# Optimization experiments

Measured on AMD Instinct MI355X. Metric: run time of the kernel, lower is better.

## Reference

```python
import jax, jax.numpy as jnp
import numpy as np

D_MODEL = 1024
N_HEADS = 16
D_K = 64
SEQ = 4096
BATCH = 1


def setup_inputs() -> dict:
    key = jax.random.key(0)
    ks = jax.random.split(key, 6)
    s = 1.0 / np.sqrt(D_MODEL)
    return {
        "h": jax.random.normal(ks[0], (BATCH, SEQ, D_MODEL), jnp.float32),
        "gamma": jnp.ones((D_MODEL,), jnp.float32),
        "beta": jnp.zeros((D_MODEL,), jnp.float32),
        "Wq": jax.random.normal(ks[1], (D_MODEL, N_HEADS * D_K), jnp.float32) * s,
        "bq": jnp.zeros((N_HEADS * D_K,), jnp.float32),
        "Wk": jax.random.normal(ks[2], (D_MODEL, N_HEADS * D_K), jnp.float32) * s,
        "bk": jnp.zeros((N_HEADS * D_K,), jnp.float32),
        "Wv": jax.random.normal(ks[3], (D_MODEL, N_HEADS * D_K), jnp.float32) * s,
        "bv": jnp.zeros((N_HEADS * D_K,), jnp.float32),
        "Wo": jax.random.normal(ks[4], (N_HEADS * D_K, D_MODEL), jnp.float32) * s,
        "bo": jnp.zeros((D_MODEL,), jnp.float32),
    }


def _rope(x):
    # x: [b, s, h, d]
    d = x.shape[-1]
    d2 = d // 2
    theta = 1.0 / (10000.0 ** (jnp.arange(0, d, 2, dtype=jnp.float32) / d))  # [d2]
    pos = jnp.arange(x.shape[1], dtype=jnp.float32)  # [s]
    idx_theta = pos[:, None] * theta[None, :]  # [s, d2]
    idx_theta2 = jnp.concatenate([idx_theta, idx_theta], axis=-1)  # [s, d]
    cos = jnp.cos(idx_theta2)[None, :, None, :]
    sin = jnp.sin(idx_theta2)[None, :, None, :]
    neg_half = jnp.concatenate([-x[..., d2:], x[..., :d2]], axis=-1)
    return x * cos + neg_half * sin


def reference(h, gamma, beta, Wq, bq, Wk, bk, Wv, bv, Wo, bo):
    b, s, dm = h.shape
    h_res = h
    # LayerNorm (eps=1e-5, matching torch default)
    mu = jnp.mean(h, axis=-1, keepdims=True)
    var = jnp.var(h, axis=-1, keepdims=True)
    hn = (h - mu) * jax.lax.rsqrt(var + 1e-5) * gamma + beta
    mh = (b, s, N_HEADS, D_K)
    q = (hn @ Wq + bq).reshape(mh)
    k = (hn @ Wk + bk).reshape(mh)
    v = (hn @ Wv + bv).reshape(mh)
    q = _rope(q)
    k = _rope(k)
    scale = 1.0 / np.sqrt(D_K)
    attn = jnp.einsum('bihd,bjhd->bhij', q, k) * scale  # [b,h,s,s]
    # causal mask
    mask = jnp.tril(jnp.ones((s, s), dtype=bool))
    attn = jnp.where(mask, attn, -jnp.inf)
    attn = jax.nn.softmax(attn, axis=-1)
    out = jnp.einsum('bhij,bjhd->bihd', attn, v).reshape(b, s, N_HEADS * D_K)
    return out @ Wo + bo + h_res
```

## Files before the change

kernel.cpp:

```cpp
#include <hip/hip_runtime.h>
#include <stdint.h>

#define SEQLEN 4096
#define DMODEL 1024
#define NHEADS 16
#define DKDIM  64

typedef unsigned short u16;
typedef unsigned int   u32;
using f32x4 = __attribute__((ext_vector_type(4))) float;
using i32x4 = __attribute__((ext_vector_type(4))) int;
using i32x2 = __attribute__((ext_vector_type(2))) int;
using u16x8 = __attribute__((ext_vector_type(8))) unsigned short;

__device__ __forceinline__ u16 f2bf(float f) {
    u32 x = __builtin_bit_cast(u32, f);
    u32 r = x + 0x7fffu + ((x >> 16) & 1u);
    return (u16)(r >> 16);
}
__device__ __forceinline__ float exp2a(float x) {
    float r; asm("v_exp_f32 %0, %1" : "=v"(r) : "v"(x)); return r;
}
__device__ __forceinline__ u32 cvtpk(float lo, float hi) {
    u32 r; asm("v_cvt_pk_bf16_f32 %0, %1, %2" : "=v"(r) : "v"(lo), "v"(hi)); return r;
}

__device__ __forceinline__ void mfma_bf16(f32x4& d, i32x4 a, i32x4 b) {
    asm("v_mfma_f32_16x16x32_bf16 %0, %1, %2, %0" : "+v"(d) : "v"(a), "v"(b));
}
__device__ __forceinline__ void mfma16_bf16(f32x4& d, i32x2 a, i32x2 b) {
    asm("v_mfma_f32_16x16x16_bf16 %0, %1, %2, %0" : "+v"(d) : "v"(a), "v"(b));
}

#define ASYNC_COPY16(gsrc, ldst) \
    __builtin_amdgcn_global_load_lds((const __attribute__((address_space(1))) void*)(gsrc), \
                                     (__attribute__((address_space(3))) void*)(ldst), 16, 0, 0)

__global__ __launch_bounds__(256) void ln_kernel(const float* __restrict__ h,
                                                 const float* __restrict__ gamma,
                                                 const float* __restrict__ beta,
                                                 u16* __restrict__ hn) {
    int row = blockIdx.x;
    int t = threadIdx.x;
    float4 v = reinterpret_cast<const float4*>(h + (size_t)row * DMODEL)[t];
    float s  = v.x + v.y + v.z + v.w;
    float s2 = v.x*v.x + v.y*v.y + v.z*v.z + v.w*v.w;
#pragma unroll
    for (int off = 1; off < 64; off <<= 1) {
        s  += __shfl_xor(s, off);
        s2 += __shfl_xor(s2, off);
    }
    __shared__ float red[8];
    int wid = t >> 6, lane = t & 63;
    if (lane == 0) { red[wid] = s; red[4 + wid] = s2; }
    __syncthreads();
    s  = red[0] + red[1] + red[2] + red[3];
    s2 = red[4] + red[5] + red[6] + red[7];
    float mu   = s * (1.0f / DMODEL);
    float rstd = rsqrtf(s2 * (1.0f / DMODEL) - mu * mu + 1e-5f);
    float4 g = reinterpret_cast<const float4*>(gamma)[t];
    float4 b = reinterpret_cast<const float4*>(beta)[t];
    ushort4 o;
    o.x = f2bf((v.x - mu) * rstd * g.x + b.x);
    o.y = f2bf((v.y - mu) * rstd * g.y + b.y);
    o.z = f2bf((v.z - mu) * rstd * g.z + b.z);
    o.w = f2bf((v.w - mu) * rstd * g.w + b.w);
    reinterpret_cast<ushort4*>(hn + (size_t)row * DMODEL)[t] = o;
}

__global__ __launch_bounds__(256) void wconv_kernel(const float* __restrict__ Wq,
                                                    const float* __restrict__ Wk,
                                                    const float* __restrict__ Wv,
                                                    const float* __restrict__ Wo,
                                                    u16* __restrict__ wqkvT,
                                                    u16* __restrict__ woT) {
    int z = blockIdx.z;
    const float* W = (z == 0) ? Wq : (z == 1) ? Wk : (z == 2) ? Wv : Wo;
    u16* Wt = (z < 3) ? wqkvT + (size_t)z * DMODEL * DMODEL : woT;
    __shared__ float tile[32][33];
    int bx = blockIdx.x * 32;
    int by = blockIdx.y * 32;
    int tx = threadIdx.x & 31, ty = threadIdx.x >> 5;
#pragma unroll
    for (int i = 0; i < 32; i += 8)
        tile[ty + i][tx] = W[(size_t)(by + ty + i) * DMODEL + bx + tx];
    __syncthreads();
#pragma unroll
    for (int i = 0; i < 32; i += 8)
        Wt[(size_t)(bx + ty + i) * DMODEL + by + tx] = f2bf(tile[tx][ty + i]);
}

__global__ void rope_table_kernel(float* __restrict__ cosT, float* __restrict__ sinT) {
    int idx = blockIdx.x * 256 + threadIdx.x;
    int s = idx >> 5, i = idx & 31;
    float theta = powf(10000.0f, -2.0f * (float)i / 64.0f);
    float ang = (float)s * theta;
    cosT[idx] = cosf(ang);
    sinT[idx] = sinf(ang);
}

template <int EPI>
__global__ __launch_bounds__(256) void gemm_kernel(const u16* __restrict__ A,
                                                   const u16* __restrict__ Bt,
                                                   const float* __restrict__ b0,
                                                   const float* __restrict__ b1,
                                                   const float* __restrict__ b2,
                                                   const float* __restrict__ resid,
                                                   const float* __restrict__ cosT,
                                                   const float* __restrict__ sinT,
                                                   u16* __restrict__ o0,
                                                   u16* __restrict__ o1,
                                                   u16* __restrict__ o2,
                                                   float* __restrict__ ofp) {
    __shared__ alignas(16) u16 As[2][128 * 64];
    __shared__ alignas(16) u16 Bs[2][128 * 64];
    int bm = blockIdx.x, bn = blockIdx.y;
    int tid = threadIdx.x;
    int wid = tid >> 6, lane = tid & 63;
    int wm = wid >> 1, wn = wid & 1;
    int t15 = lane & 15, g = lane >> 4;
    const u16* Abase = A  + (size_t)bm * 128 * DMODEL;
    const u16* Bbase = Bt + (size_t)bn * 128 * DMODEL;
    int srow = tid >> 3;
    int sslot = tid & 7;
    f32x4 acc[4][4] = {};

#define GSTAGE(b, ks)                                                                    \
    {                                                                                    \
        _Pragma("unroll")                                                                \
        for (int i = 0; i < 4; i++) {                                                    \
            int row = i * 32 + srow;                                                     \
            int col = ((sslot ^ (row & 7)) * 8) + (ks);                                  \
            ASYNC_COPY16(Abase + (size_t)row * DMODEL + col, &As[b][i * 2048 + wid * 512]); \
            ASYNC_COPY16(Bbase + (size_t)row * DMODEL + col, &Bs[b][i * 2048 + wid * 512]); \
        }                                                                                \
    }

    GSTAGE(0, 0)
    __syncthreads();
    int buf = 0;
    for (int ks = 0; ks < DMODEL; ks += 64) {
        if (ks < DMODEL - 64) GSTAGE(buf ^ 1, ks + 64)
#pragma unroll
        for (int kk = 0; kk < 2; kk++) {
            i32x4 af[4], bfr[4];
#pragma unroll
            for (int mi = 0; mi < 4; mi++) {
                int row = wm * 64 + mi * 16 + t15;
                int sl = (kk * 4 + g) ^ (row & 7);
                af[mi] = *reinterpret_cast<const i32x4*>(&As[buf][row * 64 + sl * 8]);
            }
#pragma unroll
            for (int ni = 0; ni < 4; ni++) {
                int row = wn * 64 + ni * 16 + t15;
                int sl = (kk * 4 + g) ^ (row & 7);
                bfr[ni] = *reinterpret_cast<const i32x4*>(&Bs[buf][row * 64 + sl * 8]);
            }
            __builtin_amdgcn_s_setprio(1);
#pragma unroll
            for (int mi = 0; mi < 4; mi++)
#pragma unroll
                for (int ni = 0; ni < 4; ni++)
                    mfma_bf16(acc[mi][ni], af[mi], bfr[ni]);
            __builtin_amdgcn_s_setprio(0);
        }
        __syncthreads();
        buf ^= 1;
    }
#undef GSTAGE

    if (EPI == 0) {
        int seg = bn >> 3;
        int bnl = bn & 7;
        const float* bias = (seg == 0) ? b0 : (seg == 1) ? b1 : b2;
        if (seg < 2) {
            u16* o = (seg == 0) ? o0 : o1;
            float qs = (seg == 0) ? 0.18033688f : 1.0f;
#pragma unroll
            for (int mi = 0; mi < 4; mi++) {
#pragma unroll
                for (int nl = 0; nl < 2; nl++) {
                    int n10 = bnl * 128 + wn * 64 + nl * 16 + t15;
                    int head = n10 >> 6;
                    int dA = n10 & 63, dB = dA + 32;
                    float bvA = bias[n10], bvB = bias[n10 + 32];
#pragma unroll
                    for (int r = 0; r < 4; r++) {
                        int m = bm * 128 + wm * 64 + mi * 16 + g * 4 + r;
                        float c  = cosT[m * 32 + dA];
                        float sn = sinT[m * 32 + dA];
                        float xA = acc[mi][nl][r] + bvA;
                        float xB = acc[mi][nl + 2][r] + bvB;
                        o[(size_t)(head * SEQLEN + m) * DKDIM + dA] = f2bf((xA * c - xB * sn) * qs);
                        o[(size_t)(head * SEQLEN + m) * DKDIM + dB] = f2bf((xB * c + xA * sn) * qs);
                    }
                }
            }
        } else {
#pragma unroll
            for (int mi = 0; mi < 4; mi++) {
#pragma unroll
                for (int ni = 0; ni < 4; ni++) {
                    int n10 = bnl * 128 + wn * 64 + ni * 16 + t15;
                    int head = n10 >> 6, dv = n10 & 63;
                    float bv = bias[n10];
                    int m = bm * 128 + wm * 64 + mi * 16 + g * 4;
                    ushort4 w4;
                    w4.x = f2bf(acc[mi][ni][0] + bv);
                    w4.y = f2bf(acc[mi][ni][1] + bv);
                    w4.z = f2bf(acc[mi][ni][2] + bv);
                    w4.w = f2bf(acc[mi][ni][3] + bv);
                    *reinterpret_cast<ushort4*>(&o2[(size_t)(head * DKDIM + dv) * SEQLEN + m]) = w4;
                }
            }
        }
    } else {
#pragma unroll
        for (int mi = 0; mi < 4; mi++) {
#pragma unroll
            for (int ni = 0; ni < 4; ni++) {
                int n = bn * 128 + wn * 64 + ni * 16 + t15;
                float bv = b0[n];
#pragma unroll
                for (int r = 0; r < 4; r++) {
                    int m = bm * 128 + wm * 64 + mi * 16 + g * 4 + r;
                    ofp[(size_t)m * DMODEL + n] = acc[mi][ni][r] + bv + resid[(size_t)m * DMODEL + n];
                }
            }
        }
    }
}

__global__ __launch_bounds__(512, 2) void attn_kernel(const u16* __restrict__ q,
                                                      const u16* __restrict__ k,
                                                      const u16* __restrict__ vt,
                                                      u16* __restrict__ o) {
    __shared__ alignas(16) u16 SMEM[65536];
    int bid = blockIdx.x;
    int h = bid & 15;
    int p = bid >> 4;
    int tid = threadIdx.x;
    int grp = tid >> 8;
    int wid = (tid >> 6) & 3;
    int lane = tid & 63;
    int t15 = lane & 15, g = lane >> 4;
    const u16* Qh  = q  + (size_t)h * SEQLEN * DKDIM;
    const u16* Kh  = k  + (size_t)h * SEQLEN * DKDIM;
    const u16* VtH = vt + (size_t)h * DKDIM * SEQLEN;
    int sslotK = lane & 7;
    int sslotV = lane & 15;
    float* Os  = (float*)SMEM;
    float2* Ml = (float2*)((char*)SMEM + 69632);

    int c7 = t15 & 7;
    int kc0e = t15 * 64 + ((g ^ c7) << 3);
    int kc1e = t15 * 64 + (((4 + g) ^ c7) << 3);
    int vce[8];
#pragma unroll
    for (int kb = 0; kb < 8; kb++)
        vce[kb] = t15 * 128 + ((((kb * 2) + (g >> 1)) ^ c7) << 3) + ((g & 1) << 2);

#define STAGE(bb, t_)                                                                   \
    {                                                                                   \
        int k0s = (t_) * 128;                                                           \
        u16* Kb = SMEM + (size_t)(grp * 2 + (bb)) * 8192;                               \
        u16* Vb = SMEM + 32768 + (size_t)(grp * 2 + (bb)) * 8192;                       \
        _Pragma("unroll")                                                               \
        for (int it = 0; it < 4; it++) {                                                \
            int u    = wid * 4 + it;                                                    \
            int krow = u * 8 + (lane >> 3);                                             \
            int ksl  = (sslotK ^ (krow & 7)) * 8;                                       \
            ASYNC_COPY16(Kh + (size_t)(k0s + krow) * DKDIM + ksl, Kb + u * 512);        \
            int vrow = u * 4 + (lane >> 4);                                             \
            int vsl  = (sslotV ^ (vrow & 7)) * 8;                                       \
            ASYNC_COPY16(VtH + (size_t)vrow * SEQLEN + k0s + vsl, Vb + u * 512);        \
        }                                                                               \
    }

    for (int pass = 0; pass < 2; pass++) {
        int Q = pass ? p : (31 - p);
        int n = Q + 1;
        int iters = (n + 1) >> 1;
        int q0 = Q * 128;
        int qrowA = q0 + wid * 32 + t15;
        int qrowB = qrowA + 16;
        i32x4 qfA0, qfA1, qfB0, qfB1;
        {
            const u16* qp = Qh + (size_t)qrowA * DKDIM + g * 8;
            qfA0 = *reinterpret_cast<const i32x4*>(qp);
            qfA1 = *reinterpret_cast<const i32x4*>(qp + 32);
            const u16* qp2 = qp + 16 * DKDIM;
            qfB0 = *reinterpret_cast<const i32x4*>(qp2);
            qfB1 = *reinterpret_cast<const i32x4*>(qp2 + 32);
        }
        f32x4 oA[4] = {}, oB[4] = {};
        float mA = -1e30f, mB = -1e30f, lA = 0.f, lB = 0.f;

        if (grp < n) STAGE(0, grp)
        __syncthreads();
        for (int i = 0; i < iters; i++) {
            int t = grp + 2 * i;
            bool active = t < n;
            int buf = i & 1;
            if (t + 2 < n) STAGE(buf ^ 1, t + 2)
            if (active) {
                int kbe = (grp * 2 + buf) * 8192;
                const u16* Kp0 = SMEM + kbe + kc0e;
                const u16* Kp1 = SMEM + kbe + kc1e;
                const u16* Vp  = SMEM + 32768 + kbe;
                int k0 = t * 128;
                f32x4 sA[8] = {}, sB[8] = {};
                __builtin_amdgcn_s_setprio(1);
#pragma unroll
                for (int kb = 0; kb < 8; kb++) {
                    i32x4 kf0 = *reinterpret_cast<const i32x4*>(Kp0 + kb * 1024);
                    i32x4 kf1 = *reinterpret_cast<const i32x4*>(Kp1 + kb * 1024);
                    mfma_bf16(sA[kb], kf0, qfA0);
                    mfma_bf16(sA[kb], kf1, qfA1);
                    mfma_bf16(sB[kb], kf0, qfB0);
                    mfma_bf16(sB[kb], kf1, qfB1);
                }
                __builtin_amdgcn_s_setprio(0);
                if (t == n - 1) {
#pragma unroll
                    for (int kb = 0; kb < 8; kb++)
#pragma unroll
                        for (int r = 0; r < 4; r++) {
                            int kvg = k0 + kb * 16 + g * 4 + r;
                            if (kvg > qrowA) sA[kb][r] = -1e30f;
                            if (kvg > qrowB) sB[kb][r] = -1e30f;
                        }
                }
                float amx[8], bmx[8];
#pragma unroll
                for (int kb = 0; kb < 8; kb++) {
                    amx[kb] = fmaxf(fmaxf(sA[kb][0], sA[kb][1]), fmaxf(sA[kb][2], sA[kb][3]));
                    bmx[kb] = fmaxf(fmaxf(sB[kb][0], sB[kb][1]), fmaxf(sB[kb][2], sB[kb][3]));
                }
                float mxA = fmaxf(fmaxf(fmaxf(amx[0], amx[1]), fmaxf(amx[2], amx[3])),
                                  fmaxf(fmaxf(amx[4], amx[5]), fmaxf(amx[6], amx[7])));
                float mxB = fmaxf(fmaxf(fmaxf(bmx[0], bmx[1]), fmaxf(bmx[2], bmx[3])),
                                  fmaxf(fmaxf(bmx[4], bmx[5]), fmaxf(bmx[6], bmx[7])));
                if (!__all((mxA <= mA + 8.0f) && (mxB <= mB + 8.0f))) {
                    float mrA = fmaxf(mxA, __shfl_xor(mxA, 16));
                    mrA = fmaxf(mrA, __shfl_xor(mrA, 32));
                    float mnA = fmaxf(mA, mrA);
                    float fdA = exp2a(mA - mnA);
                    mA = mnA; lA *= fdA;
                    oA[0] *= fdA; oA[1] *= fdA; oA[2] *= fdA; oA[3] *= fdA;
                    float mrB = fmaxf(mxB, __shfl_xor(mxB, 16));
                    mrB = fmaxf(mrB, __shfl_xor(mrB, 32));
                    float mnB = fmaxf(mB, mrB);
                    float fdB = exp2a(mB - mnB);
                    mB = mnB; lB *= fdB;
                    oB[0] *= fdB; oB[1] *= fdB; oB[2] *= fdB; oB[3] *= fdB;
                }
                float psA = 0.f, psB = 0.f;
                u32 pwA[16], pwB[16];
#pragma unroll
                for (int kb = 0; kb < 8; kb++) {
                    float pa0 = exp2a(sA[kb][0] - mA);
                    float pa1 = exp2a(sA[kb][1] - mA);
                    float pa2 = exp2a(sA[kb][2] - mA);
                    float pa3 = exp2a(sA[kb][3] - mA);
                    psA += (pa0 + pa1) + (pa2 + pa3);
                    pwA[kb * 2]     = cvtpk(pa0, pa1);
                    pwA[kb * 2 + 1] = cvtpk(pa2, pa3);
                    float pb0 = exp2a(sB[kb][0] - mB);
                    float pb1 = exp2a(sB[kb][1] - mB);
                    float pb2 = exp2a(sB[kb][2] - mB);
                    float pb3 = exp2a(sB[kb][3] - mB);
                    psB += (pb0 + pb1) + (pb2 + pb3);
                    pwB[kb * 2]     = cvtpk(pb0, pb1);
                    pwB[kb * 2 + 1] = cvtpk(pb2, pb3);
                }
                lA += psA;
                lB += psB;
                __builtin_amdgcn_s_setprio(1);
#pragma unroll
                for (int nb = 0; nb < 4; nb++) {
#pragma unroll
                    for (int kb = 0; kb < 8; kb++) {
                        i32x2 vf = *reinterpret_cast<const i32x2*>(Vp + vce[kb] + nb * 2048);
                        mfma16_bf16(oA[nb], vf, i32x2{(int)pwA[kb * 2], (int)pwA[kb * 2 + 1]});
                        mfma16_bf16(oB[nb], vf, i32x2{(int)pwB[kb * 2], (int)pwB[kb * 2 + 1]});
                    }
                }
                __builtin_amdgcn_s_setprio(0);
            }
            __syncthreads();
        }
        lA += __shfl_xor(lA, 16); lA += __shfl_xor(lA, 32);
        lB += __shfl_xor(lB, 16); lB += __shfl_xor(lB, 32);
        int rowA = wid * 32 + t15, rowB = rowA + 16;
#pragma unroll
        for (int nb = 0; nb < 4; nb++) {
            *reinterpret_cast<f32x4*>(&Os[(size_t)(grp * 128 + rowA) * 68 + nb * 16 + g * 4]) = oA[nb];
            *reinterpret_cast<f32x4*>(&Os[(size_t)(grp * 128 + rowB) * 68 + nb * 16 + g * 4]) = oB[nb];
        }
        if (g == 0) {
            Ml[grp * 128 + rowA] = make_float2(mA, lA);
            Ml[grp * 128 + rowB] = make_float2(mB, lB);
        }
        __syncthreads();
        {
            int r = tid >> 2, c4 = tid & 3;
            int d0 = c4 * 16;
            float2 c0 = Ml[r], c1 = Ml[128 + r];
            float M = fmaxf(c0.x, c1.x);
            float w0 = exp2a(c0.x - M), w1 = exp2a(c1.x - M);
            float invL = 1.0f / (w0 * c0.y + w1 * c1.y);
            u16* op = o + (size_t)(q0 + r) * DMODEL + h * DKDIM + d0;
#pragma unroll
            for (int j = 0; j < 2; j++) {
                f32x4 a0 = *reinterpret_cast<const f32x4*>(&Os[(size_t)r * 68 + d0 + j * 8]);
                f32x4 a1 = *reinterpret_cast<const f32x4*>(&Os[(size_t)r * 68 + d0 + j * 8 + 4]);
                f32x4 b0 = *reinterpret_cast<const f32x4*>(&Os[(size_t)(128 + r) * 68 + d0 + j * 8]);
                f32x4 b1 = *reinterpret_cast<const f32x4*>(&Os[(size_t)(128 + r) * 68 + d0 + j * 8 + 4]);
                u16x8 w8;
#pragma unroll
                for (int ii = 0; ii < 4; ii++) {
                    w8[ii]     = f2bf((w0 * a0[ii] + w1 * b0[ii]) * invL);
                    w8[4 + ii] = f2bf((w0 * a1[ii] + w1 * b1[ii]) * invL);
                }
                *reinterpret_cast<u16x8*>(op + j * 8) = w8;
            }
        }
        __syncthreads();
    }
#undef STAGE
}

extern "C" void kernel_launch(void* const* d_in, const int* in_sizes, int n_in,
                              void* d_out, int out_size, void* d_ws, size_t ws_size,
                              hipStream_t stream) {
    const float* h     = (const float*)d_in[0];
    const float* gamma = (const float*)d_in[1];
    const float* beta  = (const float*)d_in[2];
    const float* Wq    = (const float*)d_in[3];
    const float* bq    = (const float*)d_in[4];
    const float* Wk    = (const float*)d_in[5];
    const float* bk    = (const float*)d_in[6];
    const float* Wv    = (const float*)d_in[7];
    const float* bv    = (const float*)d_in[8];
    const float* Wo    = (const float*)d_in[9];
    const float* bo    = (const float*)d_in[10];
    float* out = (float*)d_out;

    char* ws = (char*)d_ws;
    u16* hn     = (u16*)(ws);
    u16* wqkvT  = (u16*)(ws + (8ull  << 20));
    u16* woT    = (u16*)(ws + (14ull << 20));
    u16* qb     = (u16*)(ws + (16ull << 20));
    u16* kbuf   = (u16*)(ws + (24ull << 20));
    u16* vtb    = (u16*)(ws + (32ull << 20));
    float* cosT = (float*)(ws + (40ull << 20));
    float* sinT = (float*)(ws + (40ull << 20) + (512ull << 10));
    u16* attn = hn;

    ln_kernel<<<SEQLEN, 256, 0, stream>>>(h, gamma, beta, hn);
    wconv_kernel<<<dim3(32, 32, 4), 256, 0, stream>>>(Wq, Wk, Wv, Wo, wqkvT, woT);
    rope_table_kernel<<<(SEQLEN * 32) / 256, 256, 0, stream>>>(cosT, sinT);
    gemm_kernel<0><<<dim3(32, 24), 256, 0, stream>>>(hn, wqkvT, bq, bk, bv, nullptr,
                                                     cosT, sinT, qb, kbuf, vtb, nullptr);
    attn_kernel<<<256, 512, 0, stream>>>(qb, kbuf, vtb, attn);
    gemm_kernel<1><<<dim3(32, 8), 256, 0, stream>>>(attn, woT, bo, nullptr, nullptr, h,
                                                    nullptr, nullptr, nullptr, nullptr, nullptr, out);
}
```

Before: 136.6 us.

## Merge prep kernels into one launch and interleave softmax with PV MFMAs

Combines the LayerNorm, weight transpose/convert and RoPE table kernels into a single prep kernel that dispatches on block index, removing two kernel launches and their serialization gaps. In the attention inner loop, each packed bf16 P fragment now feeds its PV MFMAs as soon as it is produced, instead of all exponentials finishing before any MFMA starts. This shortens the live range of the P register arrays and lets exp work overlap with matrix ops, at the cost of more frequent priority toggles and per-kb V fragment loads interleaved with ALU work.

After: 132.9 us. 1.03x faster.

```diff
diff --git a/kernel.cpp b/kernel.cpp
--- a/kernel.cpp
+++ b/kernel.cpp
@@ -36,67 +36,70 @@
     __builtin_amdgcn_global_load_lds((const __attribute__((address_space(1))) void*)(gsrc), \
                                      (__attribute__((address_space(3))) void*)(ldst), 16, 0, 0)
 
-__global__ __launch_bounds__(256) void ln_kernel(const float* __restrict__ h,
-                                                 const float* __restrict__ gamma,
-                                                 const float* __restrict__ beta,
-                                                 u16* __restrict__ hn) {
-    int row = blockIdx.x;
+__global__ __launch_bounds__(256) void prep_kernel(const float* __restrict__ Wq,
+                                                   const float* __restrict__ Wk,
+                                                   const float* __restrict__ Wv,
+                                                   const float* __restrict__ Wo,
+                                                   u16* __restrict__ wqkvT,
+                                                   u16* __restrict__ woT,
+                                                   const float* __restrict__ h,
+                                                   const float* __restrict__ gamma,
+                                                   const float* __restrict__ beta,
+                                                   u16* __restrict__ hn,
+                                                   float* __restrict__ cosT,
+                                                   float* __restrict__ sinT) {
+    __shared__ float tile[32][33];
+    __shared__ float red[8];
+    int bid = blockIdx.x;
     int t = threadIdx.x;
-    float4 v = reinterpret_cast<const float4*>(h + (size_t)row * DMODEL)[t];
-    float s  = v.x + v.y + v.z + v.w;
-    float s2 = v.x*v.x + v.y*v.y + v.z*v.z + v.w*v.w;
-#pragma unroll
-    for (int off = 1; off < 64; off <<= 1) {
-        s  += __shfl_xor(s, off);
-        s2 += __shfl_xor(s2, off);
-    }
-    __shared__ float red[8];
-    int wid = t >> 6, lane = t & 63;
-    if (lane == 0) { red[wid] = s; red[4 + wid] = s2; }
-    __syncthreads();
-    s  = red[0] + red[1] + red[2] + red[3];
-    s2 = red[4] + red[5] + red[6] + red[7];
-    float mu   = s * (1.0f / DMODEL);
-    float rstd = rsqrtf(s2 * (1.0f / DMODEL) - mu * mu + 1e-5f);
-    float4 g = reinterpret_cast<const float4*>(gamma)[t];
-    float4 b = reinterpret_cast<const float4*>(beta)[t];
-    ushort4 o;
-    o.x = f2bf((v.x - mu) * rstd * g.x + b.x);
-    o.y = f2bf((v.y - mu) * rstd * g.y + b.y);
-    o.z = f2bf((v.z - mu) * rstd * g.z + b.z);
-    o.w = f2bf((v.w - mu) * rstd * g.w + b.w);
-    reinterpret_cast<ushort4*>(hn + (size_t)row * DMODEL)[t] = o;
-}
-
-__global__ __launch_bounds__(256) void wconv_kernel(const float* __restrict__ Wq,
-                                                    const float* __restrict__ Wk,
-                                                    const float* __restrict__ Wv,
-                                                    const float* __restrict__ Wo,
-                                                    u16* __restrict__ wqkvT,
-                                                    u16* __restrict__ woT) {
-    int z = blockIdx.z;
-    const float* W = (z == 0) ? Wq : (z == 1) ? Wk : (z == 2) ? Wv : Wo;
-    u16* Wt = (z < 3) ? wqkvT + (size_t)z * DMODEL * DMODEL : woT;
-    __shared__ float tile[32][33];
-    int bx = blockIdx.x * 32;
-    int by = blockIdx.y * 32;
-    int tx = threadIdx.x & 31, ty = threadIdx.x >> 5;
-#pragma unroll
-    for (int i = 0; i < 32; i += 8)
-        tile[ty + i][tx] = W[(size_t)(by + ty + i) * DMODEL + bx + tx];
-    __syncthreads();
-#pragma unroll
-    for (int i = 0; i < 32; i += 8)
-        Wt[(size_t)(bx + ty + i) * DMODEL + by + tx] = f2bf(tile[tx][ty + i]);
-}
-
-__global__ void rope_table_kernel(float* __restrict__ cosT, float* __restrict__ sinT) {
-    int idx = blockIdx.x * 256 + threadIdx.x;
-    int s = idx >> 5, i = idx & 31;
-    float theta = powf(10000.0f, -2.0f * (float)i / 64.0f);
-    float ang = (float)s * theta;
-    cosT[idx] = cosf(ang);
-    sinT[idx] = sinf(ang);
+    if (bid < 4096) {
+        int z = bid >> 10;
+        int rem = bid & 1023;
+        const float* W = (z == 0) ? Wq : (z == 1) ? Wk : (z == 2) ? Wv : Wo;
+        u16* Wt = (z < 3) ? wqkvT + (size_t)z * DMODEL * DMODEL : woT;
+        int bx = (rem & 31) * 32;
+        int by = (rem >> 5) * 32;
+        int tx = t & 31, ty = t >> 5;
+#pragma unroll
+        for (int i = 0; i < 32; i += 8)
+            tile[ty + i][tx] = W[(size_t)(by + ty + i) * DMODEL + bx + tx];
+        __syncthreads();
+#pragma unroll
+        for (int i = 0; i < 32; i += 8)
+            Wt[(size_t)(bx + ty + i) * DMODEL + by + tx] = f2bf(tile[tx][ty + i]);
+    } else if (bid < 8192) {
+        int row = bid - 4096;
+        float4 v = reinterpret_cast<const float4*>(h + (size_t)row * DMODEL)[t];
+        float s  = v.x + v.y + v.z + v.w;
+        float s2 = v.x*v.x + v.y*v.y + v.z*v.z + v.w*v.w;
+#pragma unroll
+        for (int off = 1; off < 64; off <<= 1) {
+            s  += __shfl_xor(s, off);
+            s2 += __shfl_xor(s2, off);
+        }
+        int wid = t >> 6, lane = t & 63;
+        if (lane == 0) { red[wid] = s; red[4 + wid] = s2; }
+        __syncthreads();
+        s  = red[0] + red[1] + red[2] + red[3];
+        s2 = red[4] + red[5] + red[6] + red[7];
+        float mu   = s * (1.0f / DMODEL);
+        float rstd = rsqrtf(s2 * (1.0f / DMODEL) - mu * mu + 1e-5f);
+        float4 g = reinterpret_cast<const float4*>(gamma)[t];
+        float4 b = reinterpret_cast<const float4*>(beta)[t];
+        ushort4 o;
+        o.x = f2bf((v.x - mu) * rstd * g.x + b.x);
+        o.y = f2bf((v.y - mu) * rstd * g.y + b.y);
+        o.z = f2bf((v.z - mu) * rstd * g.z + b.z);
+        o.w = f2bf((v.w - mu) * rstd * g.w + b.w);
+        reinterpret_cast<ushort4*>(hn + (size_t)row * DMODEL)[t] = o;
+    } else {
+        int idx = (bid - 8192) * 256 + t;
+        int s = idx >> 5, i = idx & 31;
+        float theta = powf(10000.0f, -2.0f * (float)i / 64.0f);
+        float ang = (float)s * theta;
+        cosT[idx] = cosf(ang);
+        sinT[idx] = sinf(ang);
+    }
 }
 
 template <int EPI>
@@ -356,7 +359,6 @@
                     oB[0] *= fdB; oB[1] *= fdB; oB[2] *= fdB; oB[3] *= fdB;
                 }
                 float psA = 0.f, psB = 0.f;
-                u32 pwA[16], pwB[16];
 #pragma unroll
                 for (int kb = 0; kb < 8; kb++) {
                     float pa0 = exp2a(sA[kb][0] - mA);
@@ -364,29 +366,24 @@
                     float pa2 = exp2a(sA[kb][2] - mA);
                     float pa3 = exp2a(sA[kb][3] - mA);
                     psA += (pa0 + pa1) + (pa2 + pa3);
-                    pwA[kb * 2]     = cvtpk(pa0, pa1);
-                    pwA[kb * 2 + 1] = cvtpk(pa2, pa3);
+                    i32x2 pfA = i32x2{(int)cvtpk(pa0, pa1), (int)cvtpk(pa2, pa3)};
                     float pb0 = exp2a(sB[kb][0] - mB);
                     float pb1 = exp2a(sB[kb][1] - mB);
                     float pb2 = exp2a(sB[kb][2] - mB);
                     float pb3 = exp2a(sB[kb][3] - mB);
                     psB += (pb0 + pb1) + (pb2 + pb3);
-                    pwB[kb * 2]     = cvtpk(pb0, pb1);
-                    pwB[kb * 2 + 1] = cvtpk(pb2, pb3);
+                    i32x2 pfB = i32x2{(int)cvtpk(pb0, pb1), (int)cvtpk(pb2, pb3)};
+                    __builtin_amdgcn_s_setprio(1);
+#pragma unroll
+                    for (int nb = 0; nb < 4; nb++) {
+                        i32x2 vf = *reinterpret_cast<const i32x2*>(Vp + vce[kb] + nb * 2048);
+                        mfma16_bf16(oA[nb], vf, pfA);
+                        mfma16_bf16(oB[nb], vf, pfB);
+                    }
+                    __builtin_amdgcn_s_setprio(0);
                 }
                 lA += psA;
                 lB += psB;
-                __builtin_amdgcn_s_setprio(1);
-#pragma unroll
-                for (int nb = 0; nb < 4; nb++) {
-#pragma unroll
-                    for (int kb = 0; kb < 8; kb++) {
-                        i32x2 vf = *reinterpret_cast<const i32x2*>(Vp + vce[kb] + nb * 2048);
-                        mfma16_bf16(oA[nb], vf, i32x2{(int)pwA[kb * 2], (int)pwA[kb * 2 + 1]});
-                        mfma16_bf16(oB[nb], vf, i32x2{(int)pwB[kb * 2], (int)pwB[kb * 2 + 1]});
-                    }
-                }
-                __builtin_amdgcn_s_setprio(0);
             }
             __syncthreads();
         }
@@ -458,9 +455,8 @@
     float* sinT = (float*)(ws + (40ull << 20) + (512ull << 10));
     u16* attn = hn;
 
-    ln_kernel<<<SEQLEN, 256, 0, stream>>>(h, gamma, beta, hn);
-    wconv_kernel<<<dim3(32, 32, 4), 256, 0, stream>>>(Wq, Wk, Wv, Wo, wqkvT, woT);
-    rope_table_kernel<<<(SEQLEN * 32) / 256, 256, 0, stream>>>(cosT, sinT);
+    prep_kernel<<<8704, 256, 0, stream>>>(Wq, Wk, Wv, Wo, wqkvT, woT,
+                                          h, gamma, beta, hn, cosT, sinT);
     gemm_kernel<0><<<dim3(32, 24), 256, 0, stream>>>(hn, wqkvT, bq, bk, bv, nullptr,
                                                      cosT, sinT, qb, kbuf, vtb, nullptr);
     attn_kernel<<<256, 512, 0, stream>>>(qb, kbuf, vtb, attn);
```
